# Performance work log

Hardware: AMD Instinct MI355X
Metric: run time of the kernel (lower is better)

The kernel has to match this reference:

```python
import jax, jax.numpy as jnp
import numpy as np

SQRT_2_OVER_PI = 0.79788456

def gelu_tanh(x):
    # tanh-approximate GELU, matches torch F.gelu(approximate='tanh')
    return 0.5 * x * (1.0 + jnp.tanh(SQRT_2_OVER_PI * x * (1.0 + 0.044715 * x * x)))

def gelu_bwd(x):
    # analytical derivative of tanh-approx GELU (same constants as source)
    t = jnp.tanh(SQRT_2_OVER_PI * x * (1.0 + 0.044715 * x * x))
    return 0.5 * x * ((1.0 - t * t) * (SQRT_2_OVER_PI + 0.1070322243 * x * x)) + 0.5 * (1.0 + t)

def setup_inputs() -> dict:
    key = jax.random.key(0)
    ks = jax.random.split(key, 6)
    T, d_phi, d_h = 8192, 4096, 64
    d_mid = 4 * d_h
    return {
        "phi_seq": jax.random.normal(ks[0], (T, d_phi), jnp.float32),
        "C_seq": jax.random.uniform(ks[1], (T,), jnp.float32),
        "theta_K_w": jax.random.normal(ks[2], (d_h, d_phi), jnp.float32) * 0.02,
        "theta_Q_w": jax.random.normal(ks[3], (d_h, d_phi), jnp.float32) * 0.02,
        "W10": jax.random.normal(ks[4], (d_h, d_mid), jnp.float32) * 0.02,
        "b10": jnp.zeros((d_mid,), jnp.float32),
        "W20": jax.random.normal(ks[5], (d_mid,), jnp.float32) * 0.02,
        "b20": jnp.zeros((), jnp.float32),
        "log_eta": jnp.asarray(np.log(0.01), jnp.float32),
    }

def reference(phi_seq, C_seq, theta_K_w, theta_Q_w, W10, b10, W20, b20, log_eta):
    eta = jnp.exp(log_eta)
    # Slow-weight projections hoisted out of the scan (same math, one big GEMM)
    u_Q = phi_seq @ theta_Q_w.T  # [T, d_h]
    u_K = phi_seq @ theta_K_w.T  # [T, d_h]

    def step(carry, inp):
        W1, b1, W2, b2 = carry
        u_q, u_k = inp
        # score with current fast weights
        s = jax.nn.sigmoid(gelu_tanh(u_q @ W1 + b1) @ W2 + b2)
        # update fast weights (inner objective, C_t = 0.0)
        Z1 = u_k @ W1 + b1          # [d_mid]
        X2 = gelu_tanh(Z1)
        pred = jax.nn.sigmoid(X2 @ W2 + b2)
        d_Z2 = 2.0 * pred * pred * (1.0 - pred)  # d/dZ2 of (pred-0)^2
        d_Z1 = (d_Z2 * W2) * gelu_bwd(Z1)
        new_carry = (
            W1 - eta * jnp.outer(u_k, d_Z1),
            b1 - eta * d_Z1,
            W2 - eta * d_Z2 * X2,
            b2 - eta * d_Z2,
        )
        return new_carry, s

    _, scores = jax.lax.scan(step, (W10, b10, W20, b20), (u_Q, u_K))
    outer_loss = jnp.sum((scores - C_seq) ** 2)
    return scores, outer_loss
```

## Files before the change

### kernel.cpp

```cpp
#include <hip/hip_runtime.h>
#include <hip/hip_bf16.h>

#define DH 64
#define DM 256

typedef float f32x2 __attribute__((ext_vector_type(2)));

__device__ __forceinline__ f32x2 sp2(float s) { return (f32x2){s, s}; }
__device__ __forceinline__ f32x2 pkfma(f32x2 a, f32x2 b, f32x2 c) {
#if __has_builtin(__builtin_elementwise_fma)
    return __builtin_elementwise_fma(a, b, c);
#else
    f32x2 r; r.x = fmaf(a.x, b.x, c.x); r.y = fmaf(a.y, b.y, c.y); return r;
#endif
}

__device__ __forceinline__ float tanh_fast(float y) {
    float e = __expf(2.0f * y);
    return 1.0f - 2.0f / (e + 1.0f);
}
__device__ __forceinline__ float sigmoid_fast(float x) {
    return 1.0f / (1.0f + __expf(-x));
}

template <int CTRL, int RMASK>
__device__ __forceinline__ float dpp_term(float x) {
    int p = __builtin_amdgcn_update_dpp(0, __float_as_int(x), CTRL, RMASK, 0xf, false);
    return __int_as_float(p);
}
__device__ __forceinline__ float wave_sum63(float x) {
    x += dpp_term<0xB1,  0xf>(x);
    x += dpp_term<0x4E,  0xf>(x);
    x += dpp_term<0x141, 0xf>(x);
    x += dpp_term<0x140, 0xf>(x);
    x += dpp_term<0x142, 0xa>(x);
    x += dpp_term<0x143, 0xc>(x);
    return x;
}

__global__ __launch_bounds__(256) void proj_kernel(
    const float* __restrict__ phi,
    const float* __restrict__ thK,
    const float* __restrict__ thQ,
    float* __restrict__ u,
    int dphi)
{
    const int tid  = threadIdx.x;
    const int th32 = tid & 31;
    const int tt8  = tid >> 5;
    const int t0   = tt8 * 4;
    const int h0   = th32 * 4;
    const int T0   = blockIdx.x * 32;

    __shared__ float sPhiT[32][36];
    __shared__ float sThT[32][128];

    const int h   = tid >> 1;
    const int ko  = (tid & 1) * 16;
    const float* trow = (h < 64) ? (thQ + (size_t)h * dphi)
                                 : (thK + (size_t)(h - 64) * dphi);
    const int tr  = tid >> 3;
    const int k4p = (tid & 7) * 4;

    float4 pv, tv0, tv1, tv2, tv3;
    pv  = *(const float4*)&phi[(size_t)(T0 + tr) * dphi + k4p];
    tv0 = *(const float4*)&trow[ko + 0];
    tv1 = *(const float4*)&trow[ko + 4];
    tv2 = *(const float4*)&trow[ko + 8];
    tv3 = *(const float4*)&trow[ko + 12];

    float acc[4][4];
    #pragma unroll
    for (int i = 0; i < 4; ++i)
        #pragma unroll
        for (int jj = 0; jj < 4; ++jj) acc[i][jj] = 0.0f;

    const int NC = dphi / 32;
    for (int c = 0; c < NC; ++c) {
        __syncthreads();
        sPhiT[k4p + 0][tr] = pv.x;
        sPhiT[k4p + 1][tr] = pv.y;
        sPhiT[k4p + 2][tr] = pv.z;
        sPhiT[k4p + 3][tr] = pv.w;
        sThT[ko +  0][h] = tv0.x;  sThT[ko +  1][h] = tv0.y;
        sThT[ko +  2][h] = tv0.z;  sThT[ko +  3][h] = tv0.w;
        sThT[ko +  4][h] = tv1.x;  sThT[ko +  5][h] = tv1.y;
        sThT[ko +  6][h] = tv1.z;  sThT[ko +  7][h] = tv1.w;
        sThT[ko +  8][h] = tv2.x;  sThT[ko +  9][h] = tv2.y;
        sThT[ko + 10][h] = tv2.z;  sThT[ko + 11][h] = tv2.w;
        sThT[ko + 12][h] = tv3.x;  sThT[ko + 13][h] = tv3.y;
        sThT[ko + 14][h] = tv3.z;  sThT[ko + 15][h] = tv3.w;
        __syncthreads();
        if (c + 1 < NC) {
            const int kb = (c + 1) * 32;
            pv  = *(const float4*)&phi[(size_t)(T0 + tr) * dphi + kb + k4p];
            tv0 = *(const float4*)&trow[kb + ko + 0];
            tv1 = *(const float4*)&trow[kb + ko + 4];
            tv2 = *(const float4*)&trow[kb + ko + 8];
            tv3 = *(const float4*)&trow[kb + ko + 12];
        }
        #pragma unroll 8
        for (int k = 0; k < 32; ++k) {
            float4 ph = *(const float4*)&sPhiT[k][t0];
            float4 th = *(const float4*)&sThT[k][h0];
            acc[0][0] = fmaf(ph.x, th.x, acc[0][0]);
            acc[0][1] = fmaf(ph.x, th.y, acc[0][1]);
            acc[0][2] = fmaf(ph.x, th.z, acc[0][2]);
            acc[0][3] = fmaf(ph.x, th.w, acc[0][3]);
            acc[1][0] = fmaf(ph.y, th.x, acc[1][0]);
            acc[1][1] = fmaf(ph.y, th.y, acc[1][1]);
            acc[1][2] = fmaf(ph.y, th.z, acc[1][2]);
            acc[1][3] = fmaf(ph.y, th.w, acc[1][3]);
            acc[2][0] = fmaf(ph.z, th.x, acc[2][0]);
            acc[2][1] = fmaf(ph.z, th.y, acc[2][1]);
            acc[2][2] = fmaf(ph.z, th.z, acc[2][2]);
            acc[2][3] = fmaf(ph.z, th.w, acc[2][3]);
            acc[3][0] = fmaf(ph.w, th.x, acc[3][0]);
            acc[3][1] = fmaf(ph.w, th.y, acc[3][1]);
            acc[3][2] = fmaf(ph.w, th.z, acc[3][2]);
            acc[3][3] = fmaf(ph.w, th.w, acc[3][3]);
        }
    }
    #pragma unroll
    for (int i = 0; i < 4; ++i) {
        float4 o;
        o.x = acc[i][0]; o.y = acc[i][1]; o.z = acc[i][2]; o.w = acc[i][3];
        *(float4*)&u[(size_t)(T0 + t0 + i) * 128 + h0] = o;
    }
}

__global__ __launch_bounds__(256) void dots2_kernel(
    const float* __restrict__ u, float2* __restrict__ dd2, int T)
{
    const int t    = (blockIdx.x * 256 + threadIdx.x) >> 6;
    const int lane = threadIdx.x & 63;
    if (t >= T) return;
    float ukt = u[(size_t)t * 128 + 64 + lane];
    float k1 = (t >= 1) ? u[(size_t)(t - 1) * 128 + 64 + lane] : 0.f;
    float k2 = (t >= 2) ? u[(size_t)(t - 2) * 128 + 64 + lane] : 0.f;
    float p1 = k1 * ukt, p2 = k2 * ukt;
    #pragma unroll
    for (int off = 32; off > 0; off >>= 1) {
        p1 += __shfl_xor(p1, off);
        p2 += __shfl_xor(p2, off);
    }
    if (lane == 0) dd2[t] = make_float2(p1, p2);
}

__global__ __launch_bounds__(256, 1) void scan_k4(
    const float* __restrict__ u,
    const float2* __restrict__ dd2g,
    const float* __restrict__ W10,
    const float* __restrict__ b10,
    const float* __restrict__ W20,
    const float* __restrict__ b20,
    const float* __restrict__ log_eta,
    float* __restrict__ e1s,
    float* __restrict__ g2s,
    float* __restrict__ dz2s,
    int T)
{
    const int j    = threadIdx.x;
    const int lane = j & 63;
    const int wv   = j >> 6;
    const int uko  = 16 * wv;

    __shared__ __align__(16) float  ubuf[2][64][68];
    __shared__ __align__(16) float  pbuf[2][4][256];
    __shared__ __align__(16) float  ebufT[4][4][72];
    __shared__ __align__(16) float  pqk[2][4];
    __shared__ __align__(16) float2 dbuf[2][64];

    const int NB = T >> 6;
    const int sl = j >> 2, qq = j & 3;

    {
        const float* src = u + (size_t)sl * 128 + 64 + qq * 16;
        #pragma unroll
        for (int k = 0; k < 4; ++k)
            *(float4*)&ubuf[0][sl][qq * 16 + k * 4] = *(const float4*)&src[k * 4];
        if (j < 64) dbuf[0][j] = dd2g[j];
        if (j < 4)  pqk[1][j] = -2.5e29f;
        float* ez = &ebufT[2][0][0];
        for (int k = j; k < 2 * 4 * 72; k += 256) ez[k] = 0.f;
    }

    f32x2 w1p[32];
    #pragma unroll
    for (int i = 0; i < 16; ++i) {
        float4 wr = *(const float4*)&W10[(uko + i) * DM + lane * 4];
        w1p[2 * i]     = (f32x2){wr.x, wr.y};
        w1p[2 * i + 1] = (f32x2){wr.z, wr.w};
    }
    float b1j = b10[j];
    float w2j = W20[j];
    float b2  = b20[0];
    const float eta = __expf(log_eta[0]);
    float dZ2p = 0.f, en1 = 0.f, en2 = 0.f, x2p = 0.f;

    __syncthreads();

    {
        const float* ur0 = &ubuf[0][0][uko];
        f32x2 a0 = sp2(0.f), a1 = sp2(0.f);
        #pragma unroll
        for (int q = 0; q < 4; ++q) {
            float4 us = *(const float4*)&ur0[q * 4];
            a0 = pkfma(sp2(us.x), w1p[8*q+0], a0); a1 = pkfma(sp2(us.x), w1p[8*q+1], a1);
            a0 = pkfma(sp2(us.y), w1p[8*q+2], a0); a1 = pkfma(sp2(us.y), w1p[8*q+3], a1);
            a0 = pkfma(sp2(us.z), w1p[8*q+4], a0); a1 = pkfma(sp2(us.z), w1p[8*q+5], a1);
            a0 = pkfma(sp2(us.w), w1p[8*q+6], a0); a1 = pkfma(sp2(us.w), w1p[8*q+7], a1);
        }
        float4 wk; wk.x = a0.x; wk.y = a0.y; wk.z = a1.x; wk.w = a1.y;
        *(float4*)&pbuf[0][wv][lane * 4] = wk;
    }
    __syncthreads();

    float4 st[4];
    float2 std2 = make_float2(0.f, 0.f);

    for (int t = 0; t < T; ++t) {
        const int r   = t & 63;
        const int B   = t >> 6;
        const int bs  = B & 1;
        const int pbR = t & 1;

        float4 pqK = *(const float4*)&pqk[pbR ^ 1][0];
        const int sE = (t + 2) & 3;
        float eb0 = ebufT[sE][0][lane];
        float eb1 = ebufT[sE][1][lane];
        float eb2 = ebufT[sE][2][lane];
        float eb3 = ebufT[sE][3][lane];
        float2 dd = dbuf[bs][r];
        float pB0 = pbuf[pbR][0][j], pB1 = pbuf[pbR][1][j];
        float pB2 = pbuf[pbR][2][j], pB3 = pbuf[pbR][3][j];
        const int rn = (t + 1 < T) ? t + 1 : T - 1;
        const int rm = (t >= 2) ? t - 2 : 0;
        const float* urN = &ubuf[(rn >> 6) & 1][rn & 63][uko];
        const float* urM = &ubuf[(rm >> 6) & 1][rm & 63][uko];
        float4 n0 = *(const float4*)&urN[0],  n1 = *(const float4*)&urN[4];
        float4 n2 = *(const float4*)&urN[8],  n3 = *(const float4*)&urN[12];
        float4 m0 = *(const float4*)&urM[0],  m1 = *(const float4*)&urM[4];
        float4 m2 = *(const float4*)&urM[8],  m3 = *(const float4*)&urM[12];

        float zp   = ((pqK.x + pqK.y) + (pqK.z + pqK.w)) + b2;
        float pred = sigmoid_fast(zp);
        float dZ2  = 2.f * pred * pred * (1.f - pred);
        float e1o  = dZ2 * en1;
        if (t > 0) {
            e1s[(size_t)(t - 1) * 256 + j] = e1o;
            g2s[(size_t)(t - 1) * 256 + j] = dZ2 * x2p;
            if (j == 0) dz2s[t - 1] = dZ2;
        }

        f32x2 e1g0 = sp2(dZ2p) * (f32x2){eb0, eb1};
        f32x2 e1g1 = sp2(dZ2p) * (f32x2){eb2, eb3};
        f32x2 a0 = sp2(0.f), a1 = sp2(0.f);
#define ROWK(ib, ums, uns) {                                   \
        f32x2 wa = pkfma(sp2(-(ums)), e1g0, w1p[ib]);          \
        f32x2 wb = pkfma(sp2(-(ums)), e1g1, w1p[(ib) + 1]);    \
        w1p[ib] = wa; w1p[(ib) + 1] = wb;                      \
        a0 = pkfma(sp2(uns), wa, a0);                          \
        a1 = pkfma(sp2(uns), wb, a1); }
        ROWK(0,  m0.x, n0.x); ROWK(2,  m0.y, n0.y);
        ROWK(4,  m0.z, n0.z); ROWK(6,  m0.w, n0.w);
        ROWK(8,  m1.x, n1.x); ROWK(10, m1.y, n1.y);
        ROWK(12, m1.z, n1.z); ROWK(14, m1.w, n1.w);
        ROWK(16, m2.x, n2.x); ROWK(18, m2.y, n2.y);
        ROWK(20, m2.z, n2.z); ROWK(22, m2.w, n2.w);
        ROWK(24, m3.x, n3.x); ROWK(26, m3.y, n3.y);
        ROWK(28, m3.z, n3.z); ROWK(30, m3.w, n3.w);
#undef ROWK
        { float4 wk; wk.x = a0.x; wk.y = a0.y; wk.z = a1.x; wk.w = a1.y;
          *(float4*)&pbuf[pbR ^ 1][wv][lane * 4] = wk; }

        float e1o2 = dZ2p * en2;
        b1j -= e1o;
        w2j  = fmaf(-eta * dZ2, x2p, w2j);
        b2  -= eta * dZ2;
        float Pk = ((pB0 + pB1) + (pB2 + pB3));
        float zk = Pk + b1j - e1o2 * dd.y - e1o * dd.x;
        float tk = tanh_fast(0.79788456f * zk * fmaf(0.044715f, zk * zk, 1.f));
        float x2 = 0.5f * zk * (1.f + tk);
        float gb = 0.5f * zk * ((1.f - tk * tk) *
                   fmaf(0.1070322243f, zk * zk, 0.79788456f))
                 + 0.5f * (1.f + tk);
        float en = eta * w2j * gb;
        ebufT[t & 3][j & 3][j >> 2] = en;
        float pk = wave_sum63(x2 * w2j);
        if (lane == 63) pqk[t & 1][wv] = pk;

        dZ2p = dZ2; en2 = en1; en1 = en; x2p = x2;

        if (r == 0 && B + 1 < NB) {
            const float* src = u + (size_t)((B + 1) * 64 + sl) * 128 + 64 + qq * 16;
            #pragma unroll
            for (int k = 0; k < 4; ++k) st[k] = *(const float4*)&src[k * 4];
            if (j < 64) std2 = dd2g[(B + 1) * 64 + j];
        }
        if (r == 32 && B + 1 < NB) {
            #pragma unroll
            for (int k = 0; k < 4; ++k)
                *(float4*)&ubuf[bs ^ 1][sl][qq * 16 + k * 4] = st[k];
            if (j < 64) dbuf[bs ^ 1][j] = std2;
        }

        asm volatile("s_waitcnt lgkmcnt(0)" ::: "memory");
        __builtin_amdgcn_s_barrier();
        asm volatile("" ::: "memory");
    }

    {
        float4 pqK = *(const float4*)&pqk[(T - 1) & 1][0];
        float zp   = ((pqK.x + pqK.y) + (pqK.z + pqK.w)) + b2;
        float pred = sigmoid_fast(zp);
        float dZ2  = 2.f * pred * pred * (1.f - pred);
        e1s[(size_t)(T - 1) * 256 + j] = dZ2 * en1;
        g2s[(size_t)(T - 1) * 256 + j] = dZ2 * x2p;
        if (j == 0) dz2s[T - 1] = dZ2;
    }
}

__global__ __launch_bounds__(256) void delta_kernel(
    const float* __restrict__ u,
    const float* __restrict__ e1s,
    const float* __restrict__ g2s,
    const float* __restrict__ dz2s,
    float* __restrict__ snapW,
    float* __restrict__ snapB1,
    float* __restrict__ snapW2,
    float* __restrict__ snapB2)
{
    const int b  = blockIdx.x + 1;
    const int s0 = (b - 1) * 128;
    const int j  = threadIdx.x;

    __shared__ __align__(16) float uks[128][64];

    #pragma unroll
    for (int k = 0; k < 8; ++k) {
        int l = k * 256 + j;
        int s = l >> 4, q = l & 15;
        *(float4*)&uks[s][q * 4] =
            *(const float4*)&u[(size_t)(s0 + s) * 128 + 64 + q * 4];
    }
    __syncthreads();

    float acc[64];
    #pragma unroll
    for (int i = 0; i < 64; ++i) acc[i] = 0.f;
    float sB1 = 0.f, sW2 = 0.f, sB2 = 0.f;

    for (int s = 0; s < 128; ++s) {
        float e1v = e1s[(size_t)(s0 + s) * 256 + j];
        float g2v = g2s[(size_t)(s0 + s) * 256 + j];
        sB1 += e1v;
        sW2 += g2v;
        sB2 += dz2s[s0 + s];
        #pragma unroll
        for (int q = 0; q < 16; ++q) {
            float4 uv = *(const float4*)&uks[s][q * 4];
            acc[4*q+0] = fmaf(uv.x, e1v, acc[4*q+0]);
            acc[4*q+1] = fmaf(uv.y, e1v, acc[4*q+1]);
            acc[4*q+2] = fmaf(uv.z, e1v, acc[4*q+2]);
            acc[4*q+3] = fmaf(uv.w, e1v, acc[4*q+3]);
        }
    }

    float* dW = snapW + (size_t)b * 16384;
    #pragma unroll
    for (int i = 0; i < 64; ++i) dW[i * 256 + j] = acc[i];
    snapB1[b * 256 + j] = sB1;
    snapW2[b * 256 + j] = sW2;
    if (j == 0) snapB2[b] = sB2;
}

__global__ __launch_bounds__(256) void prefix_kernel(
    const float* __restrict__ W10,
    const float* __restrict__ b10,
    const float* __restrict__ W20,
    const float* __restrict__ b20,
    const float* __restrict__ log_eta,
    float* __restrict__ snapW,
    float* __restrict__ snapB1,
    float* __restrict__ snapW2,
    float* __restrict__ snapB2,
    int NS)
{
    const int i = blockIdx.x;
    const int j = threadIdx.x;
    const float eta = __expf(log_eta[0]);

    float w = W10[i * 256 + j];
    snapW[(size_t)0 * 16384 + i * 256 + j] = w;
    for (int c = 1; c < NS; ++c) {
        float d = snapW[(size_t)c * 16384 + i * 256 + j];
        w -= d;
        snapW[(size_t)c * 16384 + i * 256 + j] = w;
    }

    if (i == 0) {
        float b1 = b10[j];
        float w2 = W20[j];
        snapB1[j] = b1;
        snapW2[j] = w2;
        for (int c = 1; c < NS; ++c) {
            b1 -= snapB1[c * 256 + j];
            w2 -= eta * snapW2[c * 256 + j];
            snapB1[c * 256 + j] = b1;
            snapW2[c * 256 + j] = w2;
        }
        if (j == 0) {
            float b2 = b20[0];
            snapB2[0] = b2;
            for (int c = 1; c < NS; ++c) {
                b2 -= eta * snapB2[c];
                snapB2[c] = b2;
            }
        }
    }
}

#define TB 32
__global__ __launch_bounds__(256) void scores_kernel(
    const float* __restrict__ u,
    const float* __restrict__ e1s,
    const float* __restrict__ g2s,
    const float* __restrict__ dz2s,
    const float* __restrict__ snapW,
    const float* __restrict__ snapB1,
    const float* __restrict__ snapW2,
    const float* __restrict__ snapB2,
    const float* __restrict__ log_eta,
    float* __restrict__ out,
    int T)
{
    const int tid = threadIdx.x;
    const int t0  = blockIdx.x * TB;
    const int j   = tid;
    const int wv  = tid >> 6;
    const int lane = tid & 63;
    const int snapc = t0 >> 7;

    __shared__ __align__(16) float uq[TB][68];
    __shared__ __align__(16) float uk[TB][68];
    __shared__ __align__(16) float Dl[TB][36];
    __shared__ float redl[2][4];

    #pragma unroll
    for (int k = 0; k < 2; ++k) {
        int idx = tid * 2 + k;
        int tl = idx >> 4, c4 = idx & 15;
        *(float4*)&uq[tl][c4 * 4] = *(const float4*)&u[(size_t)(t0 + tl) * 128 + c4 * 4];
    }
    const float eta = __expf(log_eta[0]);
    float w2p = snapW2[snapc * 256 + j];
    float b2p = snapB2[snapc];
    float b1j = snapB1[snapc * 256 + j];
    __syncthreads();

    float acc[TB];
    {
        const float* Wsn = snapW + (size_t)snapc * 16384;
        float wcol[64];
        #pragma unroll
        for (int i = 0; i < 64; ++i) wcol[i] = Wsn[i * DM + j];
        for (int tl = 0; tl < TB; ++tl) {
            float a = b1j;
            #pragma unroll
            for (int q = 0; q < 16; ++q) {
                float4 uv = *(const float4*)&uq[tl][q * 4];
                a = fmaf(uv.x, wcol[4*q+0], a);
                a = fmaf(uv.y, wcol[4*q+1], a);
                a = fmaf(uv.z, wcol[4*q+2], a);
                a = fmaf(uv.w, wcol[4*q+3], a);
            }
            acc[tl] = a;
        }
    }

    const int cs = snapc << 2;
    const int ce = t0 >> 5;
    for (int c = cs; c <= ce; ++c) {
        const int sc = c * TB;
        __syncthreads();
        #pragma unroll
        for (int k = 0; k < 2; ++k) {
            int idx = tid * 2 + k;
            int sl = idx >> 4, c4 = idx & 15;
            *(float4*)&uk[sl][c4 * 4] = *(const float4*)&u[(size_t)(sc + sl) * 128 + 64 + c4 * 4];
        }
        __syncthreads();
        {
            int tl = tid & 31, sg = tid >> 5;
            float4 uqr[16];
            #pragma unroll
            for (int q = 0; q < 16; ++q) uqr[q] = *(const float4*)&uq[tl][q * 4];
            #pragma unroll
            for (int k = 0; k < 4; ++k) {
                int sl = sg * 4 + k;
                float d = 0.f;
                #pragma unroll
                for (int q = 0; q < 16; ++q) {
                    float4 ukr = *(const float4*)&uk[sl][q * 4];
                    d = fmaf(ukr.x, uqr[q].x, d);
                    d = fmaf(ukr.y, uqr[q].y, d);
                    d = fmaf(ukr.z, uqr[q].z, d);
                    d = fmaf(ukr.w, uqr[q].w, d);
                }
                Dl[sl][tl] = d;
            }
        }
        __syncthreads();

        const bool lastc = (c == ce);
        if (!lastc) {
            float e1acc = 0.f;
            for (int sl = 0; sl < TB; ++sl) {
                const int s = sc + sl;
                float e1v = e1s[(size_t)s * 256 + j];
                float g2v = g2s[(size_t)s * 256 + j];
                float dzv = dz2s[s];
                w2p = fmaf(-eta, g2v, w2p);
                b2p = fmaf(-eta, dzv, b2p);
                e1acc += e1v;
                float4 dreg[8];
                #pragma unroll
                for (int q = 0; q < 8; ++q) dreg[q] = *(const float4*)&Dl[sl][q * 4];
                #pragma unroll
                for (int tl = 0; tl < TB; ++tl) {
                    float D = (tl & 2) ? ((tl & 1) ? dreg[tl>>2].w : dreg[tl>>2].z)
                                       : ((tl & 1) ? dreg[tl>>2].y : dreg[tl>>2].x);
                    acc[tl] = fmaf(-e1v, D, acc[tl]);
                }
            }
            #pragma unroll
            for (int tl = 0; tl < TB; ++tl) acc[tl] -= e1acc;
        } else {
            for (int sl = 0; sl < TB; ++sl) {
                const int s = sc + sl;
                float zq = 0.f;
                #pragma unroll
                for (int tl = 0; tl < TB; ++tl) if (tl == sl) zq = acc[tl];
                float tq = tanh_fast(0.79788456f * zq * fmaf(0.044715f, zq*zq, 1.f));
                float aq = 0.5f * zq * (1.f + tq);
                float v  = wave_sum63(aq * w2p);
                if (lane == 63) redl[sl & 1][wv] = v;
                __syncthreads();
                float zs = redl[sl & 1][0] + redl[sl & 1][1] + redl[sl & 1][2] + redl[sl & 1][3] + b2p;
                if (tid == 0) out[t0 + sl] = sigmoid_fast(zs);

                float e1v = e1s[(size_t)s * 256 + j];
                float g2v = g2s[(size_t)s * 256 + j];
                float dzv = dz2s[s];
                w2p = fmaf(-eta, g2v, w2p);
                b2p = fmaf(-eta, dzv, b2p);
                float4 dreg[8];
                #pragma unroll
                for (int q = 0; q < 8; ++q) dreg[q] = *(const float4*)&Dl[sl][q * 4];
                #pragma unroll
                for (int tl = 0; tl < TB; ++tl) {
                    float D = (tl & 2) ? ((tl & 1) ? dreg[tl>>2].w : dreg[tl>>2].z)
                                       : ((tl & 1) ? dreg[tl>>2].y : dreg[tl>>2].x);
                    float e1m = (tl > sl) ? e1v : 0.f;
                    acc[tl] = fmaf(-e1m, D + 1.f, acc[tl]);
                }
            }
        }
    }
}

__global__ __launch_bounds__(256) void loss_kernel(
    const float* __restrict__ C, float* __restrict__ out, int T)
{
    const int tid = threadIdx.x;
    const int wv = tid >> 6, lane = tid & 63;
    __shared__ float part[4];
    float acc = 0.f;
    for (int t = tid; t < T; t += 256) {
        float d = out[t] - C[t];
        acc = fmaf(d, d, acc);
    }
    acc = wave_sum63(acc);
    if (lane == 63) part[wv] = acc;
    __syncthreads();
    if (tid == 0) out[T] = ((part[0] + part[1]) + (part[2] + part[3]));
}

extern "C" void kernel_launch(void* const* d_in, const int* in_sizes, int n_in,
                              void* d_out, int out_size, void* d_ws, size_t ws_size,
                              hipStream_t stream) {
    const float* phi     = (const float*)d_in[0];
    const float* C_seq   = (const float*)d_in[1];
    const float* thK     = (const float*)d_in[2];
    const float* thQ     = (const float*)d_in[3];
    const float* W10     = (const float*)d_in[4];
    const float* b10     = (const float*)d_in[5];
    const float* W20     = (const float*)d_in[6];
    const float* b20     = (const float*)d_in[7];
    const float* log_eta = (const float*)d_in[8];

    const int T    = in_sizes[1];
    const int dphi = in_sizes[0] / T;
    const int NS   = T >> 7;

    char* ws = (char*)d_ws;
    size_t off = 0;
    float*  uw     = (float*)(ws + off);  off += (size_t)T * 128 * 4;
    float2* dd2    = (float2*)(ws + off); off += (size_t)T * 2 * 4;
    float*  dz2s   = (float*)(ws + off);  off += (size_t)T * 4;
    float*  e1s    = (float*)(ws + off);  off += (size_t)T * 256 * 4;
    float*  g2s    = (float*)(ws + off);  off += (size_t)T * 256 * 4;
    float*  snapW  = (float*)(ws + off);  off += (size_t)NS * 16384 * 4;
    float*  snapB1 = (float*)(ws + off);  off += (size_t)NS * 256 * 4;
    float*  snapW2 = (float*)(ws + off);  off += (size_t)NS * 256 * 4;
    float*  snapB2 = (float*)(ws + off);  off += (size_t)NS * 4;

    proj_kernel<<<T / 32, 256, 0, stream>>>(phi, thK, thQ, uw, dphi);
    dots2_kernel<<<T / 4, 256, 0, stream>>>(uw, dd2, T);
    scan_k4<<<1, 256, 0, stream>>>(uw, dd2, W10, b10, W20, b20, log_eta,
                                   e1s, g2s, dz2s, T);
    delta_kernel<<<NS - 1, 256, 0, stream>>>(uw, e1s, g2s, dz2s,
                                             snapW, snapB1, snapW2, snapB2);
    prefix_kernel<<<64, 256, 0, stream>>>(W10, b10, W20, b20, log_eta,
                                          snapW, snapB1, snapW2, snapB2, NS);
    scores_kernel<<<T / TB, 256, 0, stream>>>(uw, e1s, g2s, dz2s,
                                              snapW, snapB1, snapW2, snapB2,
                                              log_eta, (float*)d_out, T);
    loss_kernel<<<1, 256, 0, stream>>>(C_seq, (float*)d_out, T);
}
```

Before: 5.450 ms.

## Split sequential scan rows across eight waves instead of four

The single-block recurrent scan kernel now runs 512 threads. Each wave owns 8 of the 64 input rows of the fast weight W1 instead of 16, halving the per-thread weight registers and the dependent FMA chain per timestep. The partial products are reduced across 8 waves through shared memory. The duplicated column threads in waves 4-7 skip the global writes and the ebuf/pqk stores. The trade-off is a wider per-step barrier, extra shared-memory partial reads and redundant scalar GELU work in the upper waves.

```diff
diff --git a/kernel.cpp b/kernel.cpp
--- a/kernel.cpp
+++ b/kernel.cpp
@@ -147,7 +147,7 @@
     if (lane == 0) dd2[t] = make_float2(p1, p2);
 }
 
-__global__ __launch_bounds__(256, 1) void scan_k4(
+__global__ __launch_bounds__(512, 1) void scan_k8(
     const float* __restrict__ u,
     const float2* __restrict__ dd2g,
     const float* __restrict__ W10,
@@ -163,37 +163,37 @@
     const int j    = threadIdx.x;
     const int lane = j & 63;
     const int wv   = j >> 6;
-    const int uko  = 16 * wv;
+    const int jcol = j & 255;
+    const int uko  = 8 * wv;
 
     __shared__ __align__(16) float  ubuf[2][64][68];
-    __shared__ __align__(16) float  pbuf[2][4][256];
+    __shared__ __align__(16) float  pbuf[2][8][256];
     __shared__ __align__(16) float  ebufT[4][4][72];
     __shared__ __align__(16) float  pqk[2][4];
     __shared__ __align__(16) float2 dbuf[2][64];
 
     const int NB = T >> 6;
-    const int sl = j >> 2, qq = j & 3;
+    const int sl = j >> 3, qq = j & 7;
 
     {
-        const float* src = u + (size_t)sl * 128 + 64 + qq * 16;
-        #pragma unroll
-        for (int k = 0; k < 4; ++k)
-            *(float4*)&ubuf[0][sl][qq * 16 + k * 4] = *(const float4*)&src[k * 4];
+        const float* src = u + (size_t)sl * 128 + 64 + qq * 8;
+        *(float4*)&ubuf[0][sl][qq * 8 + 0] = *(const float4*)&src[0];
+        *(float4*)&ubuf[0][sl][qq * 8 + 4] = *(const float4*)&src[4];
         if (j < 64) dbuf[0][j] = dd2g[j];
         if (j < 4)  pqk[1][j] = -2.5e29f;
         float* ez = &ebufT[2][0][0];
-        for (int k = j; k < 2 * 4 * 72; k += 256) ez[k] = 0.f;
-    }
-
-    f32x2 w1p[32];
-    #pragma unroll
-    for (int i = 0; i < 16; ++i) {
+        for (int k = j; k < 2 * 4 * 72; k += 512) ez[k] = 0.f;
+    }
+
+    f32x2 w1p[16];
+    #pragma unroll
+    for (int i = 0; i < 8; ++i) {
         float4 wr = *(const float4*)&W10[(uko + i) * DM + lane * 4];
         w1p[2 * i]     = (f32x2){wr.x, wr.y};
         w1p[2 * i + 1] = (f32x2){wr.z, wr.w};
     }
-    float b1j = b10[j];
-    float w2j = W20[j];
+    float b1j = b10[jcol];
+    float w2j = W20[jcol];
     float b2  = b20[0];
     const float eta = __expf(log_eta[0]);
     float dZ2p = 0.f, en1 = 0.f, en2 = 0.f, x2p = 0.f;
@@ -202,21 +202,23 @@
 
     {
         const float* ur0 = &ubuf[0][0][uko];
+        float4 us0 = *(const float4*)&ur0[0];
+        float4 us1 = *(const float4*)&ur0[4];
         f32x2 a0 = sp2(0.f), a1 = sp2(0.f);
-        #pragma unroll
-        for (int q = 0; q < 4; ++q) {
-            float4 us = *(const float4*)&ur0[q * 4];
-            a0 = pkfma(sp2(us.x), w1p[8*q+0], a0); a1 = pkfma(sp2(us.x), w1p[8*q+1], a1);
-            a0 = pkfma(sp2(us.y), w1p[8*q+2], a0); a1 = pkfma(sp2(us.y), w1p[8*q+3], a1);
-            a0 = pkfma(sp2(us.z), w1p[8*q+4], a0); a1 = pkfma(sp2(us.z), w1p[8*q+5], a1);
-            a0 = pkfma(sp2(us.w), w1p[8*q+6], a0); a1 = pkfma(sp2(us.w), w1p[8*q+7], a1);
-        }
+        a0 = pkfma(sp2(us0.x), w1p[0],  a0); a1 = pkfma(sp2(us0.x), w1p[1],  a1);
+        a0 = pkfma(sp2(us0.y), w1p[2],  a0); a1 = pkfma(sp2(us0.y), w1p[3],  a1);
+        a0 = pkfma(sp2(us0.z), w1p[4],  a0); a1 = pkfma(sp2(us0.z), w1p[5],  a1);
+        a0 = pkfma(sp2(us0.w), w1p[6],  a0); a1 = pkfma(sp2(us0.w), w1p[7],  a1);
+        a0 = pkfma(sp2(us1.x), w1p[8],  a0); a1 = pkfma(sp2(us1.x), w1p[9],  a1);
+        a0 = pkfma(sp2(us1.y), w1p[10], a0); a1 = pkfma(sp2(us1.y), w1p[11], a1);
+        a0 = pkfma(sp2(us1.z), w1p[12], a0); a1 = pkfma(sp2(us1.z), w1p[13], a1);
+        a0 = pkfma(sp2(us1.w), w1p[14], a0); a1 = pkfma(sp2(us1.w), w1p[15], a1);
         float4 wk; wk.x = a0.x; wk.y = a0.y; wk.z = a1.x; wk.w = a1.y;
         *(float4*)&pbuf[0][wv][lane * 4] = wk;
     }
     __syncthreads();
 
-    float4 st[4];
+    float4 st0, st1;
     float2 std2 = make_float2(0.f, 0.f);
 
     for (int t = 0; t < T; ++t) {
@@ -232,24 +234,24 @@
         float eb2 = ebufT[sE][2][lane];
         float eb3 = ebufT[sE][3][lane];
         float2 dd = dbuf[bs][r];
-        float pB0 = pbuf[pbR][0][j], pB1 = pbuf[pbR][1][j];
-        float pB2 = pbuf[pbR][2][j], pB3 = pbuf[pbR][3][j];
+        float pB0 = pbuf[pbR][0][jcol], pB1 = pbuf[pbR][1][jcol];
+        float pB2 = pbuf[pbR][2][jcol], pB3 = pbuf[pbR][3][jcol];
+        float pB4 = pbuf[pbR][4][jcol], pB5 = pbuf[pbR][5][jcol];
+        float pB6 = pbuf[pbR][6][jcol], pB7 = pbuf[pbR][7][jcol];
         const int rn = (t + 1 < T) ? t + 1 : T - 1;
         const int rm = (t >= 2) ? t - 2 : 0;
         const float* urN = &ubuf[(rn >> 6) & 1][rn & 63][uko];
         const float* urM = &ubuf[(rm >> 6) & 1][rm & 63][uko];
-        float4 n0 = *(const float4*)&urN[0],  n1 = *(const float4*)&urN[4];
-        float4 n2 = *(const float4*)&urN[8],  n3 = *(const float4*)&urN[12];
-        float4 m0 = *(const float4*)&urM[0],  m1 = *(const float4*)&urM[4];
-        float4 m2 = *(const float4*)&urM[8],  m3 = *(const float4*)&urM[12];
+        float4 n0 = *(const float4*)&urN[0], n1 = *(const float4*)&urN[4];
+        float4 m0 = *(const float4*)&urM[0], m1 = *(const float4*)&urM[4];
 
         float zp   = ((pqK.x + pqK.y) + (pqK.z + pqK.w)) + b2;
         float pred = sigmoid_fast(zp);
         float dZ2  = 2.f * pred * pred * (1.f - pred);
         float e1o  = dZ2 * en1;
-        if (t > 0) {
-            e1s[(size_t)(t - 1) * 256 + j] = e1o;
-            g2s[(size_t)(t - 1) * 256 + j] = dZ2 * x2p;
+        if (t > 0 && j < 256) {
+            e1s[(size_t)(t - 1) * 256 + jcol] = e1o;
+            g2s[(size_t)(t - 1) * 256 + jcol] = dZ2 * x2p;
             if (j == 0) dz2s[t - 1] = dZ2;
         }
 
@@ -266,10 +268,6 @@
         ROWK(4,  m0.z, n0.z); ROWK(6,  m0.w, n0.w);
         ROWK(8,  m1.x, n1.x); ROWK(10, m1.y, n1.y);
         ROWK(12, m1.z, n1.z); ROWK(14, m1.w, n1.w);
-        ROWK(16, m2.x, n2.x); ROWK(18, m2.y, n2.y);
-        ROWK(20, m2.z, n2.z); ROWK(22, m2.w, n2.w);
-        ROWK(24, m3.x, n3.x); ROWK(26, m3.y, n3.y);
-        ROWK(28, m3.z, n3.z); ROWK(30, m3.w, n3.w);
 #undef ROWK
         { float4 wk; wk.x = a0.x; wk.y = a0.y; wk.z = a1.x; wk.w = a1.y;
           *(float4*)&pbuf[pbR ^ 1][wv][lane * 4] = wk; }
@@ -278,7 +276,7 @@
         b1j -= e1o;
         w2j  = fmaf(-eta * dZ2, x2p, w2j);
         b2  -= eta * dZ2;
-        float Pk = ((pB0 + pB1) + (pB2 + pB3));
+        float Pk = (((pB0 + pB1) + (pB2 + pB3)) + ((pB4 + pB5) + (pB6 + pB7)));
         float zk = Pk + b1j - e1o2 * dd.y - e1o * dd.x;
         float tk = tanh_fast(0.79788456f * zk * fmaf(0.044715f, zk * zk, 1.f));
         float x2 = 0.5f * zk * (1.f + tk);
@@ -286,22 +284,21 @@
                    fmaf(0.1070322243f, zk * zk, 0.79788456f))
                  + 0.5f * (1.f + tk);
         float en = eta * w2j * gb;
-        ebufT[t & 3][j & 3][j >> 2] = en;
+        if (j < 256) ebufT[t & 3][j & 3][j >> 2] = en;
         float pk = wave_sum63(x2 * w2j);
-        if (lane == 63) pqk[t & 1][wv] = pk;
+        if (lane == 63 && wv < 4) pqk[t & 1][wv] = pk;
 
         dZ2p = dZ2; en2 = en1; en1 = en; x2p = x2;
 
         if (r == 0 && B + 1 < NB) {
-            const float* src = u + (size_t)((B + 1) * 64 + sl) * 128 + 64 + qq * 16;
-            #pragma unroll
-            for (int k = 0; k < 4; ++k) st[k] = *(const float4*)&src[k * 4];
+            const float* src = u + (size_t)((B + 1) * 64 + sl) * 128 + 64 + qq * 8;
+            st0 = *(const float4*)&src[0];
+            st1 = *(const float4*)&src[4];
             if (j < 64) std2 = dd2g[(B + 1) * 64 + j];
         }
         if (r == 32 && B + 1 < NB) {
-            #pragma unroll
-            for (int k = 0; k < 4; ++k)
-                *(float4*)&ubuf[bs ^ 1][sl][qq * 16 + k * 4] = st[k];
+            *(float4*)&ubuf[bs ^ 1][sl][qq * 8 + 0] = st0;
+            *(float4*)&ubuf[bs ^ 1][sl][qq * 8 + 4] = st1;
             if (j < 64) dbuf[bs ^ 1][j] = std2;
         }
 
@@ -315,9 +312,11 @@
         float zp   = ((pqK.x + pqK.y) + (pqK.z + pqK.w)) + b2;
         float pred = sigmoid_fast(zp);
         float dZ2  = 2.f * pred * pred * (1.f - pred);
-        e1s[(size_t)(T - 1) * 256 + j] = dZ2 * en1;
-        g2s[(size_t)(T - 1) * 256 + j] = dZ2 * x2p;
-        if (j == 0) dz2s[T - 1] = dZ2;
+        if (j < 256) {
+            e1s[(size_t)(T - 1) * 256 + jcol] = dZ2 * en1;
+            g2s[(size_t)(T - 1) * 256 + jcol] = dZ2 * x2p;
+            if (j == 0) dz2s[T - 1] = dZ2;
+        }
     }
 }
 
@@ -618,7 +617,7 @@
 
     proj_kernel<<<T / 32, 256, 0, stream>>>(phi, thK, thQ, uw, dphi);
     dots2_kernel<<<T / 4, 256, 0, stream>>>(uw, dd2, T);
-    scan_k4<<<1, 256, 0, stream>>>(uw, dd2, W10, b10, W20, b20, log_eta,
+    scan_k8<<<1, 512, 0, stream>>>(uw, dd2, W10, b10, W20, b20, log_eta,
                                    e1s, g2s, dz2s, T);
     delta_kernel<<<NS - 1, 256, 0, stream>>>(uw, e1s, g2s, dz2s,
                                              snapW, snapB1, snapW2, snapB2);
```

Result: slower. 6.143 ms (+12.7%).

## Process two timesteps per barrier in sequential scan with redundant per-wave nonlinearity

Applied to the files above, without the earlier changes.

The single-block scan now advances two timesteps per loop iteration. Dot-product corrections with the previous three keys are used so that the second step's pre-activation can be formed without a fresh matvec. Each wave redundantly computes the GELU, its derivative and the score reduction for all 256 hidden units, which removes the cross-wave e/pqk exchanges and halves the number of barriers. The cost is four times more transcendental work per thread and two matvecs per iteration, which lengthens the serial critical path of each iteration.

```diff
diff --git a/kernel.cpp b/kernel.cpp
--- a/kernel.cpp
+++ b/kernel.cpp
@@ -129,8 +129,8 @@
     }
 }
 
-__global__ __launch_bounds__(256) void dots2_kernel(
-    const float* __restrict__ u, float2* __restrict__ dd2, int T)
+__global__ __launch_bounds__(256) void dots3_kernel(
+    const float* __restrict__ u, float4* __restrict__ dd4, int T)
 {
     const int t    = (blockIdx.x * 256 + threadIdx.x) >> 6;
     const int lane = threadIdx.x & 63;
@@ -138,18 +138,20 @@
     float ukt = u[(size_t)t * 128 + 64 + lane];
     float k1 = (t >= 1) ? u[(size_t)(t - 1) * 128 + 64 + lane] : 0.f;
     float k2 = (t >= 2) ? u[(size_t)(t - 2) * 128 + 64 + lane] : 0.f;
-    float p1 = k1 * ukt, p2 = k2 * ukt;
+    float k3 = (t >= 3) ? u[(size_t)(t - 3) * 128 + 64 + lane] : 0.f;
+    float p1 = k1 * ukt, p2 = k2 * ukt, p3 = k3 * ukt;
     #pragma unroll
     for (int off = 32; off > 0; off >>= 1) {
         p1 += __shfl_xor(p1, off);
         p2 += __shfl_xor(p2, off);
-    }
-    if (lane == 0) dd2[t] = make_float2(p1, p2);
-}
-
-__global__ __launch_bounds__(256, 1) void scan_k4(
+        p3 += __shfl_xor(p3, off);
+    }
+    if (lane == 0) dd4[t] = make_float4(p1, p2, p3, 0.f);
+}
+
+__global__ __launch_bounds__(256, 1) void scan_k2(
     const float* __restrict__ u,
-    const float2* __restrict__ dd2g,
+    const float4* __restrict__ dd4g,
     const float* __restrict__ W10,
     const float* __restrict__ b10,
     const float* __restrict__ W20,
@@ -164,12 +166,11 @@
     const int lane = j & 63;
     const int wv   = j >> 6;
     const int uko  = 16 * wv;
+    const int c0   = 4 * lane;
 
     __shared__ __align__(16) float  ubuf[2][64][68];
-    __shared__ __align__(16) float  pbuf[2][4][256];
-    __shared__ __align__(16) float  ebufT[4][4][72];
-    __shared__ __align__(16) float  pqk[2][4];
-    __shared__ __align__(16) float2 dbuf[2][64];
+    __shared__ __align__(16) float  pbuf[2][2][4][256];
+    __shared__ __align__(16) float4 dbuf[2][64];
 
     const int NB = T >> 6;
     const int sl = j >> 2, qq = j & 3;
@@ -179,146 +180,232 @@
         #pragma unroll
         for (int k = 0; k < 4; ++k)
             *(float4*)&ubuf[0][sl][qq * 16 + k * 4] = *(const float4*)&src[k * 4];
-        if (j < 64) dbuf[0][j] = dd2g[j];
-        if (j < 4)  pqk[1][j] = -2.5e29f;
-        float* ez = &ebufT[2][0][0];
-        for (int k = j; k < 2 * 4 * 72; k += 256) ez[k] = 0.f;
+        if (j < 64) dbuf[0][j] = dd4g[j];
     }
 
     f32x2 w1p[32];
     #pragma unroll
     for (int i = 0; i < 16; ++i) {
-        float4 wr = *(const float4*)&W10[(uko + i) * DM + lane * 4];
+        float4 wr = *(const float4*)&W10[(uko + i) * DM + c0];
         w1p[2 * i]     = (f32x2){wr.x, wr.y};
         w1p[2 * i + 1] = (f32x2){wr.z, wr.w};
     }
-    float b1j = b10[j];
-    float w2j = W20[j];
+    float4 b14 = *(const float4*)&b10[c0];
+    f32x2 b1v0 = (f32x2){b14.x, b14.y}, b1v1 = (f32x2){b14.z, b14.w};
+    float4 w24 = *(const float4*)&W20[c0];
+    f32x2 w2v0 = (f32x2){w24.x, w24.y}, w2v1 = (f32x2){w24.z, w24.w};
     float b2  = b20[0];
     const float eta = __expf(log_eta[0]);
-    float dZ2p = 0.f, en1 = 0.f, en2 = 0.f, x2p = 0.f;
+
+    f32x2 e1m2a = sp2(0.f), e1m2b = sp2(0.f);
+    f32x2 e1m1a = sp2(0.f), e1m1b = sp2(0.f);
 
     __syncthreads();
 
+#define MVS(usp, A0, A1) {                                                   \
+        float4 ua_ = *(const float4*)&(usp)[0];                              \
+        float4 ub_ = *(const float4*)&(usp)[4];                              \
+        float4 uc_ = *(const float4*)&(usp)[8];                              \
+        float4 ud_ = *(const float4*)&(usp)[12];                             \
+        A0 = pkfma(sp2(ua_.x), w1p[0],  A0); A1 = pkfma(sp2(ua_.x), w1p[1],  A1); \
+        A0 = pkfma(sp2(ua_.y), w1p[2],  A0); A1 = pkfma(sp2(ua_.y), w1p[3],  A1); \
+        A0 = pkfma(sp2(ua_.z), w1p[4],  A0); A1 = pkfma(sp2(ua_.z), w1p[5],  A1); \
+        A0 = pkfma(sp2(ua_.w), w1p[6],  A0); A1 = pkfma(sp2(ua_.w), w1p[7],  A1); \
+        A0 = pkfma(sp2(ub_.x), w1p[8],  A0); A1 = pkfma(sp2(ub_.x), w1p[9],  A1); \
+        A0 = pkfma(sp2(ub_.y), w1p[10], A0); A1 = pkfma(sp2(ub_.y), w1p[11], A1); \
+        A0 = pkfma(sp2(ub_.z), w1p[12], A0); A1 = pkfma(sp2(ub_.z), w1p[13], A1); \
+        A0 = pkfma(sp2(ub_.w), w1p[14], A0); A1 = pkfma(sp2(ub_.w), w1p[15], A1); \
+        A0 = pkfma(sp2(uc_.x), w1p[16], A0); A1 = pkfma(sp2(uc_.x), w1p[17], A1); \
+        A0 = pkfma(sp2(uc_.y), w1p[18], A0); A1 = pkfma(sp2(uc_.y), w1p[19], A1); \
+        A0 = pkfma(sp2(uc_.z), w1p[20], A0); A1 = pkfma(sp2(uc_.z), w1p[21], A1); \
+        A0 = pkfma(sp2(uc_.w), w1p[22], A0); A1 = pkfma(sp2(uc_.w), w1p[23], A1); \
+        A0 = pkfma(sp2(ud_.x), w1p[24], A0); A1 = pkfma(sp2(ud_.x), w1p[25], A1); \
+        A0 = pkfma(sp2(ud_.y), w1p[26], A0); A1 = pkfma(sp2(ud_.y), w1p[27], A1); \
+        A0 = pkfma(sp2(ud_.z), w1p[28], A0); A1 = pkfma(sp2(ud_.z), w1p[29], A1); \
+        A0 = pkfma(sp2(ud_.w), w1p[30], A0); A1 = pkfma(sp2(ud_.w), w1p[31], A1); \
+    }
+
+#define UPDS(usp, EA, EB) {                                                  \
+        float4 ua_ = *(const float4*)&(usp)[0];                              \
+        float4 ub_ = *(const float4*)&(usp)[4];                              \
+        float4 uc_ = *(const float4*)&(usp)[8];                              \
+        float4 ud_ = *(const float4*)&(usp)[12];                             \
+        w1p[0]  = pkfma(sp2(-ua_.x), EA, w1p[0]);  w1p[1]  = pkfma(sp2(-ua_.x), EB, w1p[1]);  \
+        w1p[2]  = pkfma(sp2(-ua_.y), EA, w1p[2]);  w1p[3]  = pkfma(sp2(-ua_.y), EB, w1p[3]);  \
+        w1p[4]  = pkfma(sp2(-ua_.z), EA, w1p[4]);  w1p[5]  = pkfma(sp2(-ua_.z), EB, w1p[5]);  \
+        w1p[6]  = pkfma(sp2(-ua_.w), EA, w1p[6]);  w1p[7]  = pkfma(sp2(-ua_.w), EB, w1p[7]);  \
+        w1p[8]  = pkfma(sp2(-ub_.x), EA, w1p[8]);  w1p[9]  = pkfma(sp2(-ub_.x), EB, w1p[9]);  \
+        w1p[10] = pkfma(sp2(-ub_.y), EA, w1p[10]); w1p[11] = pkfma(sp2(-ub_.y), EB, w1p[11]); \
+        w1p[12] = pkfma(sp2(-ub_.z), EA, w1p[12]); w1p[13] = pkfma(sp2(-ub_.z), EB, w1p[13]); \
+        w1p[14] = pkfma(sp2(-ub_.w), EA, w1p[14]); w1p[15] = pkfma(sp2(-ub_.w), EB, w1p[15]); \
+        w1p[16] = pkfma(sp2(-uc_.x), EA, w1p[16]); w1p[17] = pkfma(sp2(-uc_.x), EB, w1p[17]); \
+        w1p[18] = pkfma(sp2(-uc_.y), EA, w1p[18]); w1p[19] = pkfma(sp2(-uc_.y), EB, w1p[19]); \
+        w1p[20] = pkfma(sp2(-uc_.z), EA, w1p[20]); w1p[21] = pkfma(sp2(-uc_.z), EB, w1p[21]); \
+        w1p[22] = pkfma(sp2(-uc_.w), EA, w1p[22]); w1p[23] = pkfma(sp2(-uc_.w), EB, w1p[23]); \
+        w1p[24] = pkfma(sp2(-ud_.x), EA, w1p[24]); w1p[25] = pkfma(sp2(-ud_.x), EB, w1p[25]); \
+        w1p[26] = pkfma(sp2(-ud_.y), EA, w1p[26]); w1p[27] = pkfma(sp2(-ud_.y), EB, w1p[27]); \
+        w1p[28] = pkfma(sp2(-ud_.z), EA, w1p[28]); w1p[29] = pkfma(sp2(-ud_.z), EB, w1p[29]); \
+        w1p[30] = pkfma(sp2(-ud_.w), EA, w1p[30]); w1p[31] = pkfma(sp2(-ud_.w), EB, w1p[31]); \
+    }
+
     {
-        const float* ur0 = &ubuf[0][0][uko];
-        f32x2 a0 = sp2(0.f), a1 = sp2(0.f);
         #pragma unroll
-        for (int q = 0; q < 4; ++q) {
-            float4 us = *(const float4*)&ur0[q * 4];
-            a0 = pkfma(sp2(us.x), w1p[8*q+0], a0); a1 = pkfma(sp2(us.x), w1p[8*q+1], a1);
-            a0 = pkfma(sp2(us.y), w1p[8*q+2], a0); a1 = pkfma(sp2(us.y), w1p[8*q+3], a1);
-            a0 = pkfma(sp2(us.z), w1p[8*q+4], a0); a1 = pkfma(sp2(us.z), w1p[8*q+5], a1);
-            a0 = pkfma(sp2(us.w), w1p[8*q+6], a0); a1 = pkfma(sp2(us.w), w1p[8*q+7], a1);
-        }
-        float4 wk; wk.x = a0.x; wk.y = a0.y; wk.z = a1.x; wk.w = a1.y;
-        *(float4*)&pbuf[0][wv][lane * 4] = wk;
+        for (int s = 0; s < 2; ++s) {
+            const float* us = &ubuf[0][s][uko];
+            f32x2 a0 = sp2(0.f), a1 = sp2(0.f);
+            MVS(us, a0, a1);
+            float4 wk; wk.x = a0.x; wk.y = a0.y; wk.z = a1.x; wk.w = a1.y;
+            *(float4*)&pbuf[0][s][wv][c0] = wk;
+        }
     }
     __syncthreads();
 
     float4 st[4];
-    float2 std2 = make_float2(0.f, 0.f);
-
-    for (int t = 0; t < T; ++t) {
-        const int r   = t & 63;
-        const int B   = t >> 6;
-        const int bs  = B & 1;
-        const int pbR = t & 1;
-
-        float4 pqK = *(const float4*)&pqk[pbR ^ 1][0];
-        const int sE = (t + 2) & 3;
-        float eb0 = ebufT[sE][0][lane];
-        float eb1 = ebufT[sE][1][lane];
-        float eb2 = ebufT[sE][2][lane];
-        float eb3 = ebufT[sE][3][lane];
-        float2 dd = dbuf[bs][r];
-        float pB0 = pbuf[pbR][0][j], pB1 = pbuf[pbR][1][j];
-        float pB2 = pbuf[pbR][2][j], pB3 = pbuf[pbR][3][j];
-        const int rn = (t + 1 < T) ? t + 1 : T - 1;
-        const int rm = (t >= 2) ? t - 2 : 0;
-        const float* urN = &ubuf[(rn >> 6) & 1][rn & 63][uko];
-        const float* urM = &ubuf[(rm >> 6) & 1][rm & 63][uko];
-        float4 n0 = *(const float4*)&urN[0],  n1 = *(const float4*)&urN[4];
-        float4 n2 = *(const float4*)&urN[8],  n3 = *(const float4*)&urN[12];
-        float4 m0 = *(const float4*)&urM[0],  m1 = *(const float4*)&urM[4];
-        float4 m2 = *(const float4*)&urM[8],  m3 = *(const float4*)&urM[12];
-
-        float zp   = ((pqK.x + pqK.y) + (pqK.z + pqK.w)) + b2;
-        float pred = sigmoid_fast(zp);
-        float dZ2  = 2.f * pred * pred * (1.f - pred);
-        float e1o  = dZ2 * en1;
-        if (t > 0) {
-            e1s[(size_t)(t - 1) * 256 + j] = e1o;
-            g2s[(size_t)(t - 1) * 256 + j] = dZ2 * x2p;
-            if (j == 0) dz2s[t - 1] = dZ2;
-        }
-
-        f32x2 e1g0 = sp2(dZ2p) * (f32x2){eb0, eb1};
-        f32x2 e1g1 = sp2(dZ2p) * (f32x2){eb2, eb3};
-        f32x2 a0 = sp2(0.f), a1 = sp2(0.f);
-#define ROWK(ib, ums, uns) {                                   \
-        f32x2 wa = pkfma(sp2(-(ums)), e1g0, w1p[ib]);          \
-        f32x2 wb = pkfma(sp2(-(ums)), e1g1, w1p[(ib) + 1]);    \
-        w1p[ib] = wa; w1p[(ib) + 1] = wb;                      \
-        a0 = pkfma(sp2(uns), wa, a0);                          \
-        a1 = pkfma(sp2(uns), wb, a1); }
-        ROWK(0,  m0.x, n0.x); ROWK(2,  m0.y, n0.y);
-        ROWK(4,  m0.z, n0.z); ROWK(6,  m0.w, n0.w);
-        ROWK(8,  m1.x, n1.x); ROWK(10, m1.y, n1.y);
-        ROWK(12, m1.z, n1.z); ROWK(14, m1.w, n1.w);
-        ROWK(16, m2.x, n2.x); ROWK(18, m2.y, n2.y);
-        ROWK(20, m2.z, n2.z); ROWK(22, m2.w, n2.w);
-        ROWK(24, m3.x, n3.x); ROWK(26, m3.y, n3.y);
-        ROWK(28, m3.z, n3.z); ROWK(30, m3.w, n3.w);
-#undef ROWK
-        { float4 wk; wk.x = a0.x; wk.y = a0.y; wk.z = a1.x; wk.w = a1.y;
-          *(float4*)&pbuf[pbR ^ 1][wv][lane * 4] = wk; }
-
-        float e1o2 = dZ2p * en2;
-        b1j -= e1o;
-        w2j  = fmaf(-eta * dZ2, x2p, w2j);
-        b2  -= eta * dZ2;
-        float Pk = ((pB0 + pB1) + (pB2 + pB3));
-        float zk = Pk + b1j - e1o2 * dd.y - e1o * dd.x;
-        float tk = tanh_fast(0.79788456f * zk * fmaf(0.044715f, zk * zk, 1.f));
-        float x2 = 0.5f * zk * (1.f + tk);
-        float gb = 0.5f * zk * ((1.f - tk * tk) *
-                   fmaf(0.1070322243f, zk * zk, 0.79788456f))
-                 + 0.5f * (1.f + tk);
-        float en = eta * w2j * gb;
-        ebufT[t & 3][j & 3][j >> 2] = en;
-        float pk = wave_sum63(x2 * w2j);
-        if (lane == 63) pqk[t & 1][wv] = pk;
-
-        dZ2p = dZ2; en2 = en1; en1 = en; x2p = x2;
-
-        if (r == 0 && B + 1 < NB) {
+    float4 std4 = make_float4(0.f, 0.f, 0.f, 0.f);
+    const int NIT = T >> 1;
+
+    for (int m = 0; m < NIT; ++m) {
+        const int t0 = 2 * m;
+        const int r2 = t0 & 63;
+        const int B  = t0 >> 6;
+        const int bs = B & 1;
+        const int pb = m & 1;
+
+        float4 P00 = *(const float4*)&pbuf[pb][0][0][c0];
+        float4 P01 = *(const float4*)&pbuf[pb][0][1][c0];
+        float4 P02 = *(const float4*)&pbuf[pb][0][2][c0];
+        float4 P03 = *(const float4*)&pbuf[pb][0][3][c0];
+        float4 P10 = *(const float4*)&pbuf[pb][1][0][c0];
+        float4 P11 = *(const float4*)&pbuf[pb][1][1][c0];
+        float4 P12 = *(const float4*)&pbuf[pb][1][2][c0];
+        float4 P13 = *(const float4*)&pbuf[pb][1][3][c0];
+        float4 dd0 = dbuf[bs][r2];
+        float4 dd1 = dbuf[bs][r2 + 1];
+
+        f32x2 Pa0 = (f32x2){(P00.x + P01.x) + (P02.x + P03.x),
+                            (P00.y + P01.y) + (P02.y + P03.y)};
+        f32x2 Pb0 = (f32x2){(P00.z + P01.z) + (P02.z + P03.z),
+                            (P00.w + P01.w) + (P02.w + P03.w)};
+        f32x2 zka = Pa0 + b1v0 - sp2(dd0.y) * e1m2a - sp2(dd0.x) * e1m1a;
+        f32x2 zkb = Pb0 + b1v1 - sp2(dd0.y) * e1m2b - sp2(dd0.x) * e1m1b;
+        float z0 = zka.x, z1 = zka.y, z2 = zkb.x, z3 = zkb.y;
+        float tk0 = tanh_fast(0.79788456f * z0 * fmaf(0.044715f, z0*z0, 1.f));
+        float tk1 = tanh_fast(0.79788456f * z1 * fmaf(0.044715f, z1*z1, 1.f));
+        float tk2 = tanh_fast(0.79788456f * z2 * fmaf(0.044715f, z2*z2, 1.f));
+        float tk3 = tanh_fast(0.79788456f * z3 * fmaf(0.044715f, z3*z3, 1.f));
+        f32x2 x2a0 = (f32x2){0.5f*z0*(1.f+tk0), 0.5f*z1*(1.f+tk1)};
+        f32x2 x2b0 = (f32x2){0.5f*z2*(1.f+tk2), 0.5f*z3*(1.f+tk3)};
+        float gb0 = 0.5f*z0*((1.f-tk0*tk0)*fmaf(0.1070322243f, z0*z0, 0.79788456f)) + 0.5f*(1.f+tk0);
+        float gb1 = 0.5f*z1*((1.f-tk1*tk1)*fmaf(0.1070322243f, z1*z1, 0.79788456f)) + 0.5f*(1.f+tk1);
+        float gb2 = 0.5f*z2*((1.f-tk2*tk2)*fmaf(0.1070322243f, z2*z2, 0.79788456f)) + 0.5f*(1.f+tk2);
+        float gb3 = 0.5f*z3*((1.f-tk3*tk3)*fmaf(0.1070322243f, z3*z3, 0.79788456f)) + 0.5f*(1.f+tk3);
+        f32x2 pr0 = x2a0 * w2v0;
+        pr0 = pkfma(x2b0, w2v1, pr0);
+        float red0 = wave_sum63(pr0.x + pr0.y);
+        float zp0  = __int_as_float(__builtin_amdgcn_readlane(__float_as_int(red0), 63)) + b2;
+        float pred0 = sigmoid_fast(zp0);
+        float dZ20  = 2.f * pred0 * pred0 * (1.f - pred0);
+        f32x2 ed0 = sp2(eta * dZ20);
+        f32x2 e1_0a = ed0 * w2v0 * (f32x2){gb0, gb1};
+        f32x2 e1_0b = ed0 * w2v1 * (f32x2){gb2, gb3};
+        if (wv == 0) {
+            float4 e1st; e1st.x = e1_0a.x; e1st.y = e1_0a.y; e1st.z = e1_0b.x; e1st.w = e1_0b.y;
+            *(float4*)&e1s[(size_t)t0 * 256 + c0] = e1st;
+            f32x2 g2a = sp2(dZ20) * x2a0, g2b = sp2(dZ20) * x2b0;
+            float4 g2st; g2st.x = g2a.x; g2st.y = g2a.y; g2st.z = g2b.x; g2st.w = g2b.y;
+            *(float4*)&g2s[(size_t)t0 * 256 + c0] = g2st;
+            if (j == 0) dz2s[t0] = dZ20;
+        }
+        w2v0 = pkfma(sp2(-eta * dZ20), x2a0, w2v0);
+        w2v1 = pkfma(sp2(-eta * dZ20), x2b0, w2v1);
+        b2  -= eta * dZ20;
+        b1v0 = b1v0 - e1_0a;
+        b1v1 = b1v1 - e1_0b;
+
+        f32x2 Pa1 = (f32x2){(P10.x + P11.x) + (P12.x + P13.x),
+                            (P10.y + P11.y) + (P12.y + P13.y)};
+        f32x2 Pb1 = (f32x2){(P10.z + P11.z) + (P12.z + P13.z),
+                            (P10.w + P11.w) + (P12.w + P13.w)};
+        f32x2 zka1 = Pa1 + b1v0 - sp2(dd1.z) * e1m2a - sp2(dd1.y) * e1m1a - sp2(dd1.x) * e1_0a;
+        f32x2 zkb1 = Pb1 + b1v1 - sp2(dd1.z) * e1m2b - sp2(dd1.y) * e1m1b - sp2(dd1.x) * e1_0b;
+        float y0 = zka1.x, y1 = zka1.y, y2 = zkb1.x, y3 = zkb1.y;
+        float sk0 = tanh_fast(0.79788456f * y0 * fmaf(0.044715f, y0*y0, 1.f));
+        float sk1 = tanh_fast(0.79788456f * y1 * fmaf(0.044715f, y1*y1, 1.f));
+        float sk2 = tanh_fast(0.79788456f * y2 * fmaf(0.044715f, y2*y2, 1.f));
+        float sk3 = tanh_fast(0.79788456f * y3 * fmaf(0.044715f, y3*y3, 1.f));
+        f32x2 x2a1 = (f32x2){0.5f*y0*(1.f+sk0), 0.5f*y1*(1.f+sk1)};
+        f32x2 x2b1 = (f32x2){0.5f*y2*(1.f+sk2), 0.5f*y3*(1.f+sk3)};
+        float hb0 = 0.5f*y0*((1.f-sk0*sk0)*fmaf(0.1070322243f, y0*y0, 0.79788456f)) + 0.5f*(1.f+sk0);
+        float hb1 = 0.5f*y1*((1.f-sk1*sk1)*fmaf(0.1070322243f, y1*y1, 0.79788456f)) + 0.5f*(1.f+sk1);
+        float hb2 = 0.5f*y2*((1.f-sk2*sk2)*fmaf(0.1070322243f, y2*y2, 0.79788456f)) + 0.5f*(1.f+sk2);
+        float hb3 = 0.5f*y3*((1.f-sk3*sk3)*fmaf(0.1070322243f, y3*y3, 0.79788456f)) + 0.5f*(1.f+sk3);
+        f32x2 pr1 = x2a1 * w2v0;
+        pr1 = pkfma(x2b1, w2v1, pr1);
+        float red1 = wave_sum63(pr1.x + pr1.y);
+        float zp1  = __int_as_float(__builtin_amdgcn_readlane(__float_as_int(red1), 63)) + b2;
+        float pred1 = sigmoid_fast(zp1);
+        float dZ21  = 2.f * pred1 * pred1 * (1.f - pred1);
+        f32x2 ed1 = sp2(eta * dZ21);
+        f32x2 e1_1a = ed1 * w2v0 * (f32x2){hb0, hb1};
+        f32x2 e1_1b = ed1 * w2v1 * (f32x2){hb2, hb3};
+        if (wv == 0) {
+            float4 e1st; e1st.x = e1_1a.x; e1st.y = e1_1a.y; e1st.z = e1_1b.x; e1st.w = e1_1b.y;
+            *(float4*)&e1s[(size_t)(t0 + 1) * 256 + c0] = e1st;
+            f32x2 g2a = sp2(dZ21) * x2a1, g2b = sp2(dZ21) * x2b1;
+            float4 g2st; g2st.x = g2a.x; g2st.y = g2a.y; g2st.z = g2b.x; g2st.w = g2b.y;
+            *(float4*)&g2s[(size_t)(t0 + 1) * 256 + c0] = g2st;
+            if (j == 0) dz2s[t0 + 1] = dZ21;
+        }
+        w2v0 = pkfma(sp2(-eta * dZ21), x2a1, w2v0);
+        w2v1 = pkfma(sp2(-eta * dZ21), x2b1, w2v1);
+        b2  -= eta * dZ21;
+        b1v0 = b1v0 - e1_1a;
+        b1v1 = b1v1 - e1_1b;
+
+        {
+            const int tA = (t0 >= 2) ? t0 - 2 : 0;
+            const int tB = (t0 >= 1) ? t0 - 1 : 0;
+            const float* uA = &ubuf[(tA >> 6) & 1][tA & 63][uko];
+            const float* uB = &ubuf[(tB >> 6) & 1][tB & 63][uko];
+            UPDS(uA, e1m2a, e1m2b);
+            UPDS(uB, e1m1a, e1m1b);
+            if (m + 1 < NIT) {
+                const int tN0 = t0 + 2, tN1 = t0 + 3;
+                const float* uN0 = &ubuf[(tN0 >> 6) & 1][tN0 & 63][uko];
+                const float* uN1 = &ubuf[(tN1 >> 6) & 1][tN1 & 63][uko];
+                f32x2 a0 = sp2(0.f), a1 = sp2(0.f);
+                MVS(uN0, a0, a1);
+                float4 wk; wk.x = a0.x; wk.y = a0.y; wk.z = a1.x; wk.w = a1.y;
+                *(float4*)&pbuf[pb ^ 1][0][wv][c0] = wk;
+                f32x2 c0v = sp2(0.f), c1v = sp2(0.f);
+                MVS(uN1, c0v, c1v);
+                float4 wk2; wk2.x = c0v.x; wk2.y = c0v.y; wk2.z = c1v.x; wk2.w = c1v.y;
+                *(float4*)&pbuf[pb ^ 1][1][wv][c0] = wk2;
+            }
+        }
+
+        e1m2a = e1_0a; e1m2b = e1_0b;
+        e1m1a = e1_1a; e1m1b = e1_1b;
+
+        if (r2 == 0 && B + 1 < NB) {
             const float* src = u + (size_t)((B + 1) * 64 + sl) * 128 + 64 + qq * 16;
             #pragma unroll
             for (int k = 0; k < 4; ++k) st[k] = *(const float4*)&src[k * 4];
-            if (j < 64) std2 = dd2g[(B + 1) * 64 + j];
-        }
-        if (r == 32 && B + 1 < NB) {
+            if (j < 64) std4 = dd4g[(B + 1) * 64 + j];
+        }
+        if (r2 == 32 && B + 1 < NB) {
             #pragma unroll
             for (int k = 0; k < 4; ++k)
                 *(float4*)&ubuf[bs ^ 1][sl][qq * 16 + k * 4] = st[k];
-            if (j < 64) dbuf[bs ^ 1][j] = std2;
+            if (j < 64) dbuf[bs ^ 1][j] = std4;
         }
 
         asm volatile("s_waitcnt lgkmcnt(0)" ::: "memory");
         __builtin_amdgcn_s_barrier();
         asm volatile("" ::: "memory");
     }
-
-    {
-        float4 pqK = *(const float4*)&pqk[(T - 1) & 1][0];
-        float zp   = ((pqK.x + pqK.y) + (pqK.z + pqK.w)) + b2;
-        float pred = sigmoid_fast(zp);
-        float dZ2  = 2.f * pred * pred * (1.f - pred);
-        e1s[(size_t)(T - 1) * 256 + j] = dZ2 * en1;
-        g2s[(size_t)(T - 1) * 256 + j] = dZ2 * x2p;
-        if (j == 0) dz2s[T - 1] = dZ2;
-    }
+#undef MVS
+#undef UPDS
 }
 
 __global__ __launch_bounds__(256) void delta_kernel(
@@ -607,7 +694,7 @@
     char* ws = (char*)d_ws;
     size_t off = 0;
     float*  uw     = (float*)(ws + off);  off += (size_t)T * 128 * 4;
-    float2* dd2    = (float2*)(ws + off); off += (size_t)T * 2 * 4;
+    float4* dd4    = (float4*)(ws + off); off += (size_t)T * 4 * 4;
     float*  dz2s   = (float*)(ws + off);  off += (size_t)T * 4;
     float*  e1s    = (float*)(ws + off);  off += (size_t)T * 256 * 4;
     float*  g2s    = (float*)(ws + off);  off += (size_t)T * 256 * 4;
@@ -617,8 +704,8 @@
     float*  snapB2 = (float*)(ws + off);  off += (size_t)NS * 4;
 
     proj_kernel<<<T / 32, 256, 0, stream>>>(phi, thK, thQ, uw, dphi);
-    dots2_kernel<<<T / 4, 256, 0, stream>>>(uw, dd2, T);
-    scan_k4<<<1, 256, 0, stream>>>(uw, dd2, W10, b10, W20, b20, log_eta,
+    dots3_kernel<<<T / 4, 256, 0, stream>>>(uw, dd4, T);
+    scan_k2<<<1, 256, 0, stream>>>(uw, dd4, W10, b10, W20, b20, log_eta,
                                    e1s, g2s, dz2s, T);
     delta_kernel<<<NS - 1, 256, 0, stream>>>(uw, e1s, g2s, dz2s,
                                              snapW, snapB1, snapW2, snapB2);
```

Result: slower. 5.908 ms (+8.4%).
